# Kernel tuning notes

Measured on AMD Instinct MI355X. Metric: run time of the kernel, lower is better.

The kernel has to match this reference:

```python
import jax, jax.numpy as jnp
import numpy as np

BETA = 0.25
EPS = 1e-12


def l2_normalize(x, axis=-1, eps=EPS):
    return x * jax.lax.rsqrt((x * x).sum(axis=axis, keepdims=True) + eps)


def setup_inputs() -> dict:
    key = jax.random.key(0)
    k1, k2 = jax.random.split(key)
    z = jax.random.normal(k1, (16, 32, 32, 256), dtype=jnp.float32)
    # embedding_init = uniform(2.0, -1.0) -> U[-1, 1)
    embedding = jax.random.uniform(k2, (8192, 256), dtype=jnp.float32) * 2.0 - 1.0
    return {"z": z, "embedding": embedding}


def reference(z, embedding):
    e_dim = embedding.shape[-1]
    z_flat = jnp.reshape(z, (-1, e_dim))                      # [N, D]
    z_flat_n = l2_normalize(z_flat, axis=-1)                  # [N, D]
    emb_n = l2_normalize(embedding, axis=-1)                  # [K, D]
    # squared L2 distance between normalized vectors
    d = (jnp.sum(z_flat_n ** 2, axis=1, keepdims=True)
         + jnp.sum(emb_n ** 2, axis=1)
         - 2.0 * jnp.einsum('nd,kd->nk', z_flat_n, emb_n))    # [N, K]
    min_idx = jnp.reshape(jnp.argmin(d, axis=1), z.shape[:-1])  # [B,H,W]
    # codebook lookup + renormalize
    z_q = l2_normalize(jnp.take(embedding, min_idx, axis=0), axis=-1)  # [B,H,W,D]
    z_norm = l2_normalize(z, axis=-1)
    loss = (BETA * jnp.mean(jnp.square(jax.lax.stop_gradient(z_q) - z_norm))
            + jnp.mean(jnp.square(z_q - jax.lax.stop_gradient(z_norm))))
    # straight-through estimator
    z_q_st = z + jax.lax.stop_gradient(z_q - z)
    return (z_q_st, loss, min_idx)
```

## Files before the change

kernel.cpp:

```cpp
#include <hip/hip_runtime.h>
#include <math.h>

#define D 256
#define NROW 16384
#define KCODE 8192
#define MARGIN 1.2e-3f

typedef _Float16 half8 __attribute__((ext_vector_type(8)));
typedef _Float16 half4f __attribute__((ext_vector_type(4)));
typedef __attribute__((ext_vector_type(4))) float f32x4;

__device__ __forceinline__ float dot4(float4 a, float4 b) {
  return a.x * b.x + a.y * b.y + a.z * b.z + a.w * b.w;
}
__device__ __forceinline__ float wave_sum(float s) {
#pragma unroll
  for (int off = 32; off; off >>= 1) s += __shfl_xor(s, off, 64);
  return s;
}
__device__ __forceinline__ float wave_min_f(float v) {
#pragma unroll
  for (int off = 32; off; off >>= 1) v = fminf(v, __shfl_xor(v, off, 64));
  return v;
}
__device__ __forceinline__ void async16(const void* g, void* l) {
  __builtin_amdgcn_global_load_lds(
      (const __attribute__((address_space(1))) unsigned int*)g,
      (__attribute__((address_space(3))) unsigned int*)l, 16, 0, 0);
}

__global__ __launch_bounds__(256) void k_prep(const float* __restrict__ emb,
                                              const float* __restrict__ z,
                                              float* __restrict__ emb_n,
                                              float* __restrict__ e2,
                                              _Float16* __restrict__ Bb,
                                              _Float16* __restrict__ Ab) {
  const int b = blockIdx.x;
  const int w = threadIdx.x >> 6, l = threadIdx.x & 63;
  if (b < 2048) {
    int row = b * 4 + w;
    float4 v = ((const float4*)(emb + (size_t)row * D))[l];
    float s = wave_sum(dot4(v, v));
    float inv = 1.0f / sqrtf(s + 1e-12f);
    v.x *= inv; v.y *= inv; v.z *= inv; v.w *= inv;
    ((float4*)(emb_n + (size_t)row * D))[l] = v;
    float s2 = wave_sum(dot4(v, v));
    if (l == 0) e2[row] = s2;
    half4f h;
    h[0] = (_Float16)v.x; h[1] = (_Float16)v.y;
    h[2] = (_Float16)v.z; h[3] = (_Float16)v.w;
    *(half4f*)(Bb + (size_t)row * 256 + 4 * l) = h;
  } else {
    int row = (b - 2048) * 4 + w;
    float4 v = ((const float4*)(z + (size_t)row * D))[l];
    float s = wave_sum(dot4(v, v));
    float inv = 1.0f / sqrtf(s + 1e-12f);
    v.x *= inv; v.y *= inv; v.z *= inv; v.w *= inv;
    half4f h;
    h[0] = (_Float16)v.x; h[1] = (_Float16)v.y;
    h[2] = (_Float16)v.z; h[3] = (_Float16)v.w;
    *(half4f*)(Ab + (size_t)row * 256 + 4 * l) = h;
  }
}

__device__ __forceinline__ void merge2(float& d1, int& k1, float& d2, int& k2,
                                       float od1, int ok1, float od2, int ok2) {
  bool w1 = (od1 < d1) || (od1 == d1 && ok1 < k1);
  float n1 = w1 ? od1 : d1; int nk1 = w1 ? ok1 : k1;
  float c  = w1 ? d1 : od1; int ck  = w1 ? k1 : ok1;
  float c2 = w1 ? od2 : d2; int ck2 = w1 ? ok2 : k2;
  bool w2 = (c2 < c) || (c2 == c && ck2 < ck);
  d1 = n1; k1 = nk1;
  d2 = w2 ? c2 : c; k2 = w2 ? ck2 : ck;
}

__global__ __launch_bounds__(256, 2) void k_gemm_argmin7(
    const _Float16* __restrict__ Cb,
    const _Float16* __restrict__ Zb,
    const float* __restrict__ e2, float4* __restrict__ top2) {
  __shared__ _Float16 As[2 * 128 * 64];
  __shared__ _Float16 Bs[2 * 128 * 64];
  const int tid = threadIdx.x, w = tid >> 6, l = tid & 63;
  const int wm = w >> 1, wn = w & 1;
  const int quad = l >> 4, col = l & 15;
  const int xcd = blockIdx.x & 7;
  const int j = blockIdx.x >> 3;
  const int ct = xcd * 8 + (j & 7);
  const int zt = j >> 3;
  const int c0 = ct * 128;
  const size_t z0 = (size_t)zt * 128;

  const int srow = tid >> 3, su = tid & 7;
  const int g = su ^ (srow & 7);
  const _Float16* gA = Cb + ((size_t)c0 + srow) * 256 + g * 8;
  const _Float16* gB = Zb + (z0 + srow) * 256 + g * 8;
  char* dA = (char*)As + srow * 128 + su * 16;
  char* dB = (char*)Bs + srow * 128 + su * 16;

  f32x4 acc[4][4] = {};
  const int ub = col & 7;

  float e2r[16];
#pragma unroll
  for (int mf = 0; mf < 4; ++mf)
#pragma unroll
    for (int v = 0; v < 4; ++v)
      e2r[mf * 4 + v] = e2[c0 + wm * 64 + mf * 16 + quad * 4 + v];

#pragma unroll
  for (int p = 0; p < 4; ++p) {
    async16(gA + (size_t)p * 32 * 256, dA + p * 4096);
    async16(gB + (size_t)p * 32 * 256, dB + p * 4096);
  }
  asm volatile("s_waitcnt vmcnt(0)" ::: "memory");
  __builtin_amdgcn_s_barrier();
  __builtin_amdgcn_sched_barrier(0);

#pragma unroll
  for (int s = 0; s < 4; ++s) {
    const int cur = (s & 1) * 16384;
    if (s < 3) {
      const int nxt = ((s + 1) & 1) * 16384;
      const int k0 = (s + 1) * 64;
#pragma unroll
      for (int p = 0; p < 4; ++p) {
        async16(gA + (size_t)p * 32 * 256 + k0, dA + nxt + p * 4096);
        async16(gB + (size_t)p * 32 * 256 + k0, dB + nxt + p * 4096);
      }
    }
#pragma unroll
    for (int par = 0; par < 2; ++par) {
      const int uoff = (((par * 4 + quad) ^ ub) << 4);
      half8 af[4], bf[4];
#pragma unroll
      for (int mf = 0; mf < 4; ++mf)
        af[mf] = *(const half8*)((const char*)As + cur + (wm * 64 + mf * 16 + col) * 128 + uoff);
#pragma unroll
      for (int nf = 0; nf < 4; ++nf)
        bf[nf] = *(const half8*)((const char*)Bs + cur + (wn * 64 + nf * 16 + col) * 128 + uoff);
      __builtin_amdgcn_s_setprio(1);
#pragma unroll
      for (int mf = 0; mf < 4; ++mf)
#pragma unroll
        for (int nf = 0; nf < 4; ++nf)
          acc[mf][nf] = __builtin_amdgcn_mfma_f32_16x16x32_f16(af[mf], bf[nf], acc[mf][nf], 0, 0, 0);
      __builtin_amdgcn_s_setprio(0);
    }
    if (s < 3) {
      asm volatile("s_waitcnt vmcnt(0)" ::: "memory");
      __builtin_amdgcn_s_barrier();
      __builtin_amdgcn_sched_barrier(0);
    }
  }

  float4* mbuf = (float4*)As;
#pragma unroll
  for (int nf = 0; nf < 4; ++nf) {
    float d1 = 1e30f, d2 = 1e30f; int k1 = 0, k2 = 0;
#pragma unroll
    for (int mf = 0; mf < 4; ++mf)
#pragma unroll
      for (int v = 0; v < 4; ++v) {
        float d = fmaf(-2.0f, acc[mf][nf][v], e2r[mf * 4 + v]);
        int kc = c0 + wm * 64 + mf * 16 + quad * 4 + v;
        bool lt1 = d < d1, lt2 = d < d2;
        d2 = lt1 ? d1 : (lt2 ? d : d2);
        k2 = lt1 ? k1 : (lt2 ? kc : k2);
        d1 = lt1 ? d : d1;
        k1 = lt1 ? kc : k1;
      }
#pragma unroll
    for (int m = 16; m < 64; m <<= 1) {
      float od1 = __shfl_xor(d1, m, 64); int ok1 = __shfl_xor(k1, m, 64);
      float od2 = __shfl_xor(d2, m, 64); int ok2 = __shfl_xor(k2, m, 64);
      merge2(d1, k1, d2, k2, od1, ok1, od2, ok2);
    }
    if (quad == 0)
      mbuf[(wm * 2 + wn) * 64 + nf * 16 + col] =
          make_float4(d1, d2, __int_as_float(k1), __int_as_float(k2));
  }
  __syncthreads();
  if (tid < 128) {
    const int wnn = tid >> 6, zc = tid & 63;
    float4 a = mbuf[(0 * 2 + wnn) * 64 + zc];
    float4 b = mbuf[(1 * 2 + wnn) * 64 + zc];
    float d1 = a.x, d2 = a.y; int k1 = __float_as_int(a.z), k2 = __float_as_int(a.w);
    merge2(d1, k1, d2, k2, b.x, __float_as_int(b.z), b.y, __float_as_int(b.w));
    top2[((size_t)zt * 64 + ct) * 128 + tid] =
        make_float4(d1, d2, __int_as_float(k1), __int_as_float(k2));
  }
}

__global__ __launch_bounds__(256) void k_refine_gather(
    const float* __restrict__ z, const float* __restrict__ emb_n,
    const float* __restrict__ e2, const float4* __restrict__ top2,
    float* __restrict__ out0, float* __restrict__ idx_out,
    float* __restrict__ lsum, int* __restrict__ wl_row,
    unsigned long long* __restrict__ wl_mask, double* __restrict__ wl_best,
    int* __restrict__ wl_bk, int* __restrict__ n_flag) {
  __shared__ float zr[4][D];
  __shared__ float4 t2s[4][64];
  const int t = threadIdx.x;
  const int w = t >> 6, l = t & 63;
  const int row = blockIdx.x * 4 + w;
  float4 zv = ((const float4*)(z + (size_t)row * D))[l];
  float s = wave_sum(dot4(zv, zv));
  float inv = 1.0f / sqrtf(s + 1e-12f);
  float4 zn = make_float4(zv.x * inv, zv.y * inv, zv.z * inv, zv.w * inv);
  ((float4*)zr[w])[l] = zn;
  {
    const int zt = (blockIdx.x * 4) >> 7;
    const int rb = (blockIdx.x * 4) & 127;
    t2s[t & 3][t >> 2] = top2[((size_t)zt * 64 + (t >> 2)) * 128 + rb + (t & 3)];
  }
  __syncthreads();

  float4 e = t2s[w][l];
  const float ad1 = e.x, ad2 = e.y;
  const int ck1 = __float_as_int(e.z), ck2 = __float_as_int(e.w);
  const float d1g = wave_min_f(ad1);
  const float win = d1g + 2.0f * MARGIN;

  double best = 1e300; int bk = 0x7fffffff;
  unsigned long long m1 = __ballot(ad1 <= win);
  unsigned long long m2 = __ballot(ad2 <= win);
#pragma unroll 1
  for (int slot = 0; slot < 2; ++slot) {
    unsigned long long mm = slot ? m2 : m1;
    while (mm) {
      int ln = __builtin_ctzll(mm); mm &= mm - 1;
      int k = __shfl(slot ? ck2 : ck1, ln, 64);
      float4 e4 = ((const float4*)(emb_n + (size_t)k * D))[l];
      float4 z4 = ((const float4*)zr[w])[l];
      double p = (double)e4.x * (double)z4.x + (double)e4.y * (double)z4.y +
                 (double)e4.z * (double)z4.z + (double)e4.w * (double)z4.w;
#pragma unroll
      for (int off = 32; off; off >>= 1) p += __shfl_xor(p, off, 64);
      double dd = (double)e2[k] - 2.0 * p;
      if (dd < best || (dd == best && k < bk)) { best = dd; bk = k; }
    }
  }
  float4 q = ((const float4*)(emb_n + (size_t)bk * D))[l];
  float4 o;
  o.x = zv.x + (q.x - zv.x); o.y = zv.y + (q.y - zv.y);
  o.z = zv.z + (q.z - zv.z); o.w = zv.w + (q.w - zv.w);
  ((float4*)(out0 + (size_t)row * D))[l] = o;
  float dx = q.x - zn.x, dy = q.y - zn.y, dz = q.z - zn.z, dw = q.w - zn.w;
  float lp = wave_sum(dx * dx + dy * dy + dz * dz + dw * dw);
  if (l == 0) {
    lsum[row] = lp;
    idx_out[row] = (float)bk;
    if (m2) {
      int p = atomicAdd(n_flag, 1);
      wl_row[p] = row; wl_mask[p] = m2; wl_best[p] = best; wl_bk[p] = bk;
    }
  }
}

__global__ __launch_bounds__(256) void k_rescan(
    const float* __restrict__ z, const float* __restrict__ emb_n,
    const float* __restrict__ e2, const int* __restrict__ wl_row,
    const unsigned long long* __restrict__ wl_mask,
    const double* __restrict__ wl_best, const int* __restrict__ wl_bk,
    const int* __restrict__ n_flag, float* __restrict__ idx_out,
    float* __restrict__ out0, float* __restrict__ lsum) {
  __shared__ float zr[D];
  __shared__ double ph[128];
  __shared__ double sd[4];
  __shared__ int si[4];
  __shared__ int s_bk;
  const int tid = threadIdx.x;
  const int nf = *n_flag;
  for (int wi = blockIdx.x; wi < nf; wi += gridDim.x) {
    const int row = wl_row[wi];
    unsigned long long mask = wl_mask[wi];
    __syncthreads();
    if (tid < 64) {
      float4 zv = ((const float4*)(z + (size_t)row * D))[tid];
      float s = wave_sum(dot4(zv, zv));
      float inv = 1.0f / sqrtf(s + 1e-12f);
      ((float4*)zr)[tid] = make_float4(zv.x * inv, zv.y * inv, zv.z * inv, zv.w * inv);
    }
    __syncthreads();
    double best = wl_best[wi]; int bk = wl_bk[wi];
    while (mask) {
      const int sl = __builtin_ctzll(mask); mask &= mask - 1;
      const int code = (sl << 7) + (tid & 127);
      const int half = tid >> 7;
      const float4* ev = (const float4*)(emb_n + (size_t)code * D) + half * 32;
      const float4* zf = ((const float4*)zr) + half * 32;
      double a0 = 0.0, a1 = 0.0;
#pragma unroll 8
      for (int i = 0; i < 32; i += 2) {
        float4 e0 = ev[i], e1 = ev[i + 1], z0 = zf[i], z1 = zf[i + 1];
        a0 += (double)e0.x * (double)z0.x + (double)e0.y * (double)z0.y +
              (double)e0.z * (double)z0.z + (double)e0.w * (double)z0.w;
        a1 += (double)e1.x * (double)z1.x + (double)e1.y * (double)z1.y +
              (double)e1.z * (double)z1.z + (double)e1.w * (double)z1.w;
      }
      double p = a0 + a1;
      if (half) ph[tid & 127] = p;
      __syncthreads();
      if (!half) {
        double dd = (double)e2[code] - 2.0 * (p + ph[tid]);
        if (dd < best || (dd == best && code < bk)) { best = dd; bk = code; }
      }
      __syncthreads();
    }
#pragma unroll
    for (int off = 32; off; off >>= 1) {
      double od = __shfl_xor(best, off, 64); int ok = __shfl_xor(bk, off, 64);
      if (od < best || (od == best && ok < bk)) { best = od; bk = ok; }
    }
    if ((tid & 63) == 0) { sd[tid >> 6] = best; si[tid >> 6] = bk; }
    __syncthreads();
    if (tid == 0) {
#pragma unroll
      for (int q = 1; q < 4; ++q)
        if (sd[q] < best || (sd[q] == best && si[q] < bk)) { best = sd[q]; bk = si[q]; }
      s_bk = bk;
      idx_out[row] = (float)bk;
    }
    __syncthreads();
    const int fk = s_bk;
    if (tid < 64) {
      float4 zv = ((const float4*)(z + (size_t)row * D))[tid];
      float4 zn = ((const float4*)zr)[tid];
      float4 q = ((const float4*)(emb_n + (size_t)fk * D))[tid];
      float4 o;
      o.x = zv.x + (q.x - zv.x); o.y = zv.y + (q.y - zv.y);
      o.z = zv.z + (q.z - zv.z); o.w = zv.w + (q.w - zv.w);
      ((float4*)(out0 + (size_t)row * D))[tid] = o;
      float dx = q.x - zn.x, dy = q.y - zn.y, dz = q.z - zn.z, dw = q.w - zn.w;
      float lp = wave_sum(dx * dx + dy * dy + dz * dz + dw * dw);
      if (tid == 0) lsum[row] = lp;
    }
  }
}

__global__ __launch_bounds__(256) void k_reduce(const float* __restrict__ lsum,
                                                float* __restrict__ loss_out,
                                                float inv_cnt) {
  __shared__ float ws4[4];
  float s = 0.0f;
  const float4* p = (const float4*)lsum;
  for (int i = threadIdx.x; i < NROW / 4; i += 256) {
    float4 v = p[i];
    s += (v.x + v.y) + (v.z + v.w);
  }
  s = wave_sum(s);
  if ((threadIdx.x & 63) == 0) ws4[threadIdx.x >> 6] = s;
  __syncthreads();
  if (threadIdx.x == 0) {
    float m = ((ws4[0] + ws4[1]) + (ws4[2] + ws4[3])) * inv_cnt;
    *loss_out = 0.25f * m + m;
  }
}

__device__ __forceinline__ int sw_f(int row, int d4) { return row * D + 4 * (d4 ^ (row & 7)); }
__global__ __launch_bounds__(256, 1) void k_argmin_f32(const float* __restrict__ z,
                                                       const float* __restrict__ emb_n,
                                                       const float* __restrict__ e2,
                                                       float* __restrict__ idx_out, int K) {
  extern __shared__ float smem[];
  float* zs = smem; float* es = smem + 64 * D;
  int tid = threadIdx.x; int w = tid >> 6, l = tid & 63;
  size_t r0 = (size_t)blockIdx.x * 64;
#pragma unroll
  for (int i = 0; i < 16; ++i) {
    int row = 4 * i + w;
    float4 v = ((const float4*)(z + (r0 + row) * D))[l];
    float s = wave_sum(dot4(v, v));
    float inv = 1.0f / sqrtf(s + 1e-12f);
    v.x *= inv; v.y *= inv; v.z *= inv; v.w *= inv;
    *(float4*)(&zs[sw_f(row, l)]) = v;
  }
  __syncthreads();
  int tc = tid & 15, tr = tid >> 4;
  float bestd[4] = {1e30f, 1e30f, 1e30f, 1e30f};
  int bestk[4] = {0, 0, 0, 0};
  for (int k0 = 0; k0 < K; k0 += 64) {
#pragma unroll
    for (int i = 0; i < 16; ++i) {
      int row = 4 * i + w;
      float4 v = ((const float4*)(emb_n + (size_t)(k0 + row) * D))[l];
      *(float4*)(&es[sw_f(row, l)]) = v;
    }
    __syncthreads();
    float acc[4][4] = {};
#pragma unroll 4
    for (int d4 = 0; d4 < 64; ++d4) {
      float4 zv[4], ev[4];
#pragma unroll
      for (int i = 0; i < 4; ++i) zv[i] = *(const float4*)(&zs[sw_f(tr + 16 * i, d4)]);
#pragma unroll
      for (int jx = 0; jx < 4; ++jx) ev[jx] = *(const float4*)(&es[sw_f(tc + 16 * jx, d4)]);
#pragma unroll
      for (int i = 0; i < 4; ++i)
#pragma unroll
        for (int jx = 0; jx < 4; ++jx)
          acc[i][jx] = fmaf(zv[i].x, ev[jx].x, fmaf(zv[i].y, ev[jx].y,
                       fmaf(zv[i].z, ev[jx].z, fmaf(zv[i].w, ev[jx].w, acc[i][jx]))));
    }
#pragma unroll
    for (int jx = 0; jx < 4; ++jx) {
      int k = k0 + tc + 16 * jx;
      float ek = e2[k];
#pragma unroll
      for (int i = 0; i < 4; ++i) {
        float dd = fmaf(-2.0f, acc[i][jx], ek);
        if (dd < bestd[i]) { bestd[i] = dd; bestk[i] = k; }
      }
    }
    __syncthreads();
  }
#pragma unroll
  for (int i = 0; i < 4; ++i) {
    float dd = bestd[i]; int kkk = bestk[i];
#pragma unroll
    for (int off = 1; off < 16; off <<= 1) {
      float od = __shfl_xor(dd, off, 64); int ok = __shfl_xor(kkk, off, 64);
      if (od < dd || (od == dd && ok < kkk)) { dd = od; kkk = ok; }
    }
    if (tc == 0) idx_out[r0 + tr + 16 * i] = (float)kkk;
  }
}

__global__ __launch_bounds__(256) void k_gather(const float* __restrict__ z,
                                                const float* __restrict__ emb_n,
                                                const float* __restrict__ idx_f,
                                                float* __restrict__ out0,
                                                float* __restrict__ loss_acc) {
  __shared__ float wsum[4];
  int w = threadIdx.x >> 6, l = threadIdx.x & 63;
  int row = blockIdx.x * 4 + w;
  float4 zv = ((const float4*)(z + (size_t)row * D))[l];
  float s = wave_sum(dot4(zv, zv));
  float inv = 1.0f / sqrtf(s + 1e-12f);
  int k = (int)idx_f[row];
  float4 q = ((const float4*)(emb_n + (size_t)k * D))[l];
  float4 o;
  o.x = zv.x + (q.x - zv.x); o.y = zv.y + (q.y - zv.y);
  o.z = zv.z + (q.z - zv.z); o.w = zv.w + (q.w - zv.w);
  ((float4*)(out0 + (size_t)row * D))[l] = o;
  float dx = q.x - zv.x * inv, dy = q.y - zv.y * inv;
  float dz = q.z - zv.z * inv, dw = q.w - zv.w * inv;
  float lp = wave_sum(dx * dx + dy * dy + dz * dz + dw * dw);
  if (l == 0) wsum[w] = lp;
  __syncthreads();
  if (threadIdx.x == 0) atomicAdd(loss_acc, wsum[0] + wsum[1] + wsum[2] + wsum[3]);
}

__global__ void k_final(const float* __restrict__ loss_acc,
                        float* __restrict__ loss_out, float inv_cnt) {
  float m = *loss_acc * inv_cnt;
  *loss_out = 0.25f * m + m;
}

extern "C" void kernel_launch(void* const* d_in, const int* in_sizes, int n_in,
                              void* d_out, int out_size, void* d_ws, size_t ws_size,
                              hipStream_t stream) {
  const float* z = (const float*)d_in[0];
  const float* emb = (const float*)d_in[1];
  int N = in_sizes[0] / D;
  int K = in_sizes[1] / D;

  float* out0 = (float*)d_out;
  float* loss_out = out0 + (size_t)N * D;
  float* idx_out = loss_out + 1;

  char* ws = (char*)d_ws;
  float* emb_n = (float*)ws;
  float* e2 = (float*)(ws + 8388608);
  float* loss_acc = (float*)(ws + 8421376);
  int* n_flag = (int*)(ws + 8421380);
  float* lsum = (float*)(ws + 8421392);
  _Float16* Bb = (_Float16*)(ws + 8486928);
  _Float16* Ab = (_Float16*)(ws + 12681232);
  float4* top2 = (float4*)(ws + 21069840);
  const size_t NEED = 37847056;
  int* wl_row = (int*)Ab;
  unsigned long long* wl_mask = (unsigned long long*)((char*)Ab + 65536);
  double* wl_best = (double*)((char*)Ab + 196608);
  int* wl_bk = (int*)((char*)Ab + 327680);

  const float inv_cnt = 1.0f / (float)((size_t)N * D);
  hipMemsetAsync(loss_acc, 0, 8, stream);
  if (ws_size >= NEED) {
    k_prep<<<K / 4 + N / 4, 256, 0, stream>>>(emb, z, emb_n, e2, Bb, Ab);
    k_gemm_argmin7<<<(K / 128) * (N / 128), 256, 0, stream>>>(Bb, Ab, e2, top2);
    k_refine_gather<<<N / 4, 256, 0, stream>>>(z, emb_n, e2, top2, out0, idx_out,
                                               lsum, wl_row, wl_mask, wl_best,
                                               wl_bk, n_flag);
    k_rescan<<<1024, 256, 0, stream>>>(z, emb_n, e2, wl_row, wl_mask, wl_best,
                                       wl_bk, n_flag, idx_out, out0, lsum);
    k_reduce<<<1, 256, 0, stream>>>(lsum, loss_out, inv_cnt);
  } else {
    k_prep<<<K / 4 + N / 4, 256, 0, stream>>>(emb, z, emb_n, e2, Bb, Ab);
    k_argmin_f32<<<N / 64, 256, 131072, stream>>>(z, emb_n, e2, idx_out, K);
    k_gather<<<N / 4, 256, 0, stream>>>(z, emb_n, idx_out, out0, loss_acc);
    k_final<<<1, 1, 0, stream>>>(loss_acc, loss_out, inv_cnt);
  }
}
```

Before: 232.5 us.

## Load GEMM B operand directly from global into registers, drop its LDS buffer

The GEMM-argmin kernel no longer stages the Z tile through shared memory. Each lane loads its MFMA B fragments straight from global memory into registers, double-buffered across k-steps, while the codebook tile stays in LDS. This halves LDS use so occupancy can go from 2 to 3 blocks per CU, and it removes the LDS reads for B. The costs are redundant global loads of B across the two wm waves, more register pressure, and looser vmcnt waits that depend on the exact order of the loads.

Measured after the change: 252.6 us. 8.6% more time.

```diff
diff --git a/kernel.cpp b/kernel.cpp
--- a/kernel.cpp
+++ b/kernel.cpp
@@ -74,12 +74,11 @@
   d2 = w2 ? c2 : c; k2 = w2 ? ck2 : ck;
 }
 
-__global__ __launch_bounds__(256, 2) void k_gemm_argmin7(
+__global__ __launch_bounds__(256, 3) void k_gemm_argmin9(
     const _Float16* __restrict__ Cb,
     const _Float16* __restrict__ Zb,
     const float* __restrict__ e2, float4* __restrict__ top2) {
   __shared__ _Float16 As[2 * 128 * 64];
-  __shared__ _Float16 Bs[2 * 128 * 64];
   const int tid = threadIdx.x, w = tid >> 6, l = tid & 63;
   const int wm = w >> 1, wn = w & 1;
   const int quad = l >> 4, col = l & 15;
@@ -93,65 +92,93 @@
   const int srow = tid >> 3, su = tid & 7;
   const int g = su ^ (srow & 7);
   const _Float16* gA = Cb + ((size_t)c0 + srow) * 256 + g * 8;
-  const _Float16* gB = Zb + (z0 + srow) * 256 + g * 8;
   char* dA = (char*)As + srow * 128 + su * 16;
-  char* dB = (char*)Bs + srow * 128 + su * 16;
+
+  const _Float16* gB = Zb + (z0 + wn * 64 + col) * 256 + quad * 8;
 
   f32x4 acc[4][4] = {};
   const int ub = col & 7;
 
-  float e2r[16];
-#pragma unroll
-  for (int mf = 0; mf < 4; ++mf)
-#pragma unroll
-    for (int v = 0; v < 4; ++v)
-      e2r[mf * 4 + v] = e2[c0 + wm * 64 + mf * 16 + quad * 4 + v];
-
-#pragma unroll
-  for (int p = 0; p < 4; ++p) {
+  half8 bpA[4], bpB[4], bp1[4];
+
+#pragma unroll
+  for (int p = 0; p < 4; ++p)
     async16(gA + (size_t)p * 32 * 256, dA + p * 4096);
-    async16(gB + (size_t)p * 32 * 256, dB + p * 4096);
-  }
-  asm volatile("s_waitcnt vmcnt(0)" ::: "memory");
+  __builtin_amdgcn_sched_barrier(0);
+#pragma unroll
+  for (int nf = 0; nf < 4; ++nf)
+    bpA[nf] = *(const half8*)(gB + nf * 4096);
+  __builtin_amdgcn_sched_barrier(0);
+  asm volatile("s_waitcnt vmcnt(4)" ::: "memory");
   __builtin_amdgcn_s_barrier();
   __builtin_amdgcn_sched_barrier(0);
 
-#pragma unroll
-  for (int s = 0; s < 4; ++s) {
+  auto kstep = [&](int s, half8 (&bcur)[4], half8 (&bnxt)[4]) {
     const int cur = (s & 1) * 16384;
     if (s < 3) {
       const int nxt = ((s + 1) & 1) * 16384;
       const int k0 = (s + 1) * 64;
 #pragma unroll
-      for (int p = 0; p < 4; ++p) {
+      for (int p = 0; p < 4; ++p)
         async16(gA + (size_t)p * 32 * 256 + k0, dA + nxt + p * 4096);
-        async16(gB + (size_t)p * 32 * 256 + k0, dB + nxt + p * 4096);
-      }
-    }
-#pragma unroll
-    for (int par = 0; par < 2; ++par) {
-      const int uoff = (((par * 4 + quad) ^ ub) << 4);
-      half8 af[4], bf[4];
+    }
+    __builtin_amdgcn_sched_barrier(0);
+#pragma unroll
+    for (int nf = 0; nf < 4; ++nf)
+      bp1[nf] = *(const half8*)(gB + nf * 4096 + s * 64 + 32);
+    if (s < 3) {
+#pragma unroll
+      for (int nf = 0; nf < 4; ++nf)
+        bnxt[nf] = *(const half8*)(gB + nf * 4096 + (s + 1) * 64);
+    }
+    __builtin_amdgcn_sched_barrier(0);
+    {
+      const int uoff = ((quad ^ ub) << 4);
+      half8 af[4];
 #pragma unroll
       for (int mf = 0; mf < 4; ++mf)
         af[mf] = *(const half8*)((const char*)As + cur + (wm * 64 + mf * 16 + col) * 128 + uoff);
-#pragma unroll
-      for (int nf = 0; nf < 4; ++nf)
-        bf[nf] = *(const half8*)((const char*)Bs + cur + (wn * 64 + nf * 16 + col) * 128 + uoff);
       __builtin_amdgcn_s_setprio(1);
 #pragma unroll
       for (int mf = 0; mf < 4; ++mf)
 #pragma unroll
         for (int nf = 0; nf < 4; ++nf)
-          acc[mf][nf] = __builtin_amdgcn_mfma_f32_16x16x32_f16(af[mf], bf[nf], acc[mf][nf], 0, 0, 0);
+          acc[mf][nf] = __builtin_amdgcn_mfma_f32_16x16x32_f16(af[mf], bcur[nf], acc[mf][nf], 0, 0, 0);
       __builtin_amdgcn_s_setprio(0);
     }
+    {
+      const int uoff = (((4 + quad) ^ ub) << 4);
+      half8 af[4];
+#pragma unroll
+      for (int mf = 0; mf < 4; ++mf)
+        af[mf] = *(const half8*)((const char*)As + cur + (wm * 64 + mf * 16 + col) * 128 + uoff);
+      __builtin_amdgcn_s_setprio(1);
+#pragma unroll
+      for (int mf = 0; mf < 4; ++mf)
+#pragma unroll
+        for (int nf = 0; nf < 4; ++nf)
+          acc[mf][nf] = __builtin_amdgcn_mfma_f32_16x16x32_f16(af[mf], bp1[nf], acc[mf][nf], 0, 0, 0);
+      __builtin_amdgcn_s_setprio(0);
+    }
     if (s < 3) {
-      asm volatile("s_waitcnt vmcnt(0)" ::: "memory");
+      asm volatile("s_waitcnt vmcnt(8)" ::: "memory");
       __builtin_amdgcn_s_barrier();
       __builtin_amdgcn_sched_barrier(0);
     }
-  }
+  };
+  kstep(0, bpA, bpB);
+  kstep(1, bpB, bpA);
+  kstep(2, bpA, bpB);
+  kstep(3, bpB, bpA);
+
+  __syncthreads();
+
+  float e2r[16];
+#pragma unroll
+  for (int mf = 0; mf < 4; ++mf)
+#pragma unroll
+    for (int v = 0; v < 4; ++v)
+      e2r[mf * 4 + v] = e2[c0 + wm * 64 + mf * 16 + quad * 4 + v];
 
   float4* mbuf = (float4*)As;
 #pragma unroll
@@ -488,7 +515,7 @@
   hipMemsetAsync(loss_acc, 0, 8, stream);
   if (ws_size >= NEED) {
     k_prep<<<K / 4 + N / 4, 256, 0, stream>>>(emb, z, emb_n, e2, Bb, Ab);
-    k_gemm_argmin7<<<(K / 128) * (N / 128), 256, 0, stream>>>(Bb, Ab, e2, top2);
+    k_gemm_argmin9<<<(K / 128) * (N / 128), 256, 0, stream>>>(Bb, Ab, e2, top2);
     k_refine_gather<<<N / 4, 256, 0, stream>>>(z, emb_n, e2, top2, out0, idx_out,
                                                lsum, wl_row, wl_mask, wl_best,
                                                wl_bk, n_flag);
```
